# Kernel tuning notes

Hardware: AMD Instinct MI355X
Metric: run time of the kernel (lower is better)

Reference implementation:

```python
import jax, jax.numpy as jnp
import numpy as np

VOCAB, EMBED, HIDDEN, NUM_CLASSES, PAD_IDX = 50257, 128, 128, 4, 0
B, T = 256, 512


def setup_inputs() -> dict:
    key = jax.random.key(0)
    ks = jax.random.split(key, 10)
    x = jax.random.randint(ks[0], (B, T), 0, VOCAB)
    h0 = jnp.zeros((B, HIDDEN), dtype=jnp.float32)
    # embedding: uniform(-0.1, 0.1), pad row zeroed (matches init_weights)
    emb = jax.random.uniform(ks[1], (VOCAB, EMBED), jnp.float32, -0.1, 0.1)
    emb = emb.at[PAD_IDX].set(0.0)
    def xavier(k, shape):
        fan_out, fan_in = shape
        bound = float(np.sqrt(6.0 / (fan_in + fan_out)))
        return jax.random.uniform(k, shape, jnp.float32, -bound, bound)
    W_ih = xavier(ks[2], (HIDDEN, EMBED))      # rnn.weight_ih_l0
    W_hh = xavier(ks[3], (HIDDEN, HIDDEN))     # rnn.weight_hh_l0
    b_ih = jnp.zeros((HIDDEN,), jnp.float32)
    b_hh = jnp.zeros((HIDDEN,), jnp.float32)
    W1 = xavier(ks[4], (2 * HIDDEN, HIDDEN))   # output_layer1
    b1 = jnp.zeros((2 * HIDDEN,), jnp.float32)
    W2 = xavier(ks[5], (NUM_CLASSES, 2 * HIDDEN))  # output_layer2
    b2 = jnp.zeros((NUM_CLASSES,), jnp.float32)
    return {"x": x, "h0": h0, "emb": emb, "W_ih": W_ih, "W_hh": W_hh,
            "b_ih": b_ih, "b_hh": b_hh, "W1": W1, "b1": b1, "W2": W2, "b2": b2}


def reference(x, h0, emb, W_ih, W_hh, b_ih, b_hh, W1, b1, W2, b2):
    # Embedding lookup (dropout layers are identity in eval mode)
    embedded = emb[x]                                    # [B, T, E]
    # Precompute input projection for every step, then scan the recurrence.
    x_proj = jnp.einsum('bte,he->bth', embedded, W_ih) + b_ih + b_hh  # [B, T, H]
    x_proj_t = jnp.swapaxes(x_proj, 0, 1)                # [T, B, H]

    def step(h, xp):
        h_new = jnp.tanh(xp + h @ W_hh.T)                # [B, H]
        return h_new, None

    last_hidden, _ = jax.lax.scan(step, h0, x_proj_t)    # [B, H]
    # MLP head: Linear -> ReLU -> Linear
    hidden_mlp = jax.nn.relu(last_hidden @ W1.T + b1)    # [B, 2H]
    logits = hidden_mlp @ W2.T + b2                      # [B, C]
    return (logits, last_hidden)
```

## Files before the change

kernel.cpp:

```cpp
#include <hip/hip_runtime.h>
#include <hip/hip_bf16.h>
#include <math.h>

#define BB 256
#define TT 512
#define EE 128
#define HH 128
#define NC 4
#define MM (BB * TT)

typedef __bf16 bf16x8 __attribute__((ext_vector_type(8)));
typedef __bf16 bf16x4 __attribute__((ext_vector_type(4)));
typedef float  f32x4  __attribute__((ext_vector_type(4)));
typedef float  f32x2  __attribute__((ext_vector_type(2)));

__device__ __forceinline__ float fast_tanh(float x) {
    float t = __builtin_amdgcn_exp2f(x * 2.885390081777927f);
    return 1.f - 2.f * __builtin_amdgcn_rcpf(1.f + t);
}

template <typename XPT>
__global__ __launch_bounds__(256, 2) void embed_gemm(
    const int* __restrict__ x, const float* __restrict__ emb,
    const float* __restrict__ Wih, const float* __restrict__ bih,
    const float* __restrict__ bhh, XPT* __restrict__ xpout)
{
    const int tid = threadIdx.x;
    const int m0  = blockIdx.x * 128;

    const int LDA = 72;
    __shared__ __bf16 Ah[128 * 72];
    __shared__ __bf16 Al[128 * 72];
    __shared__ __bf16 Wh[128 * 72];
    __shared__ __bf16 Wl[128 * 72];
    __shared__ float  bias_s[128];
    __shared__ int    gix[128];

    if (tid < 128) {
        gix[tid]    = x[m0 + tid];
        bias_s[tid] = bih[tid] + bhh[tid];
    }

    const int lane = tid & 63, wid = tid >> 6;
    const int col  = lane & 15, quad = lane >> 4;

    f32x4 acc[2][8];
#pragma unroll
    for (int mt = 0; mt < 2; ++mt)
#pragma unroll
        for (int nt = 0; nt < 8; ++nt) acc[mt][nt] = f32x4{0.f, 0.f, 0.f, 0.f};

    __syncthreads();

#pragma unroll
    for (int half = 0; half < 2; ++half) {
#pragma unroll
        for (int it = 0; it < 8; ++it) {
            int c   = it * 256 + tid;
            int row = c >> 4;
            int seg = c & 15;

            float4 wv = ((const float4*)Wih)[row * 32 + half * 16 + seg];
            bf16x4 wh, wl;
            wh[0] = (__bf16)wv.x; wl[0] = (__bf16)(wv.x - (float)wh[0]);
            wh[1] = (__bf16)wv.y; wl[1] = (__bf16)(wv.y - (float)wh[1]);
            wh[2] = (__bf16)wv.z; wl[2] = (__bf16)(wv.z - (float)wh[2]);
            wh[3] = (__bf16)wv.w; wl[3] = (__bf16)(wv.w - (float)wh[3]);
            *(bf16x4*)&Wh[row * LDA + seg * 4] = wh;
            *(bf16x4*)&Wl[row * LDA + seg * 4] = wl;

            int gi = gix[row];
            float4 av = ((const float4*)emb)[(size_t)gi * 32 + half * 16 + seg];
            bf16x4 ah, al;
            ah[0] = (__bf16)av.x; al[0] = (__bf16)(av.x - (float)ah[0]);
            ah[1] = (__bf16)av.y; al[1] = (__bf16)(av.y - (float)ah[1]);
            ah[2] = (__bf16)av.z; al[2] = (__bf16)(av.z - (float)ah[2]);
            ah[3] = (__bf16)av.w; al[3] = (__bf16)(av.w - (float)ah[3]);
            *(bf16x4*)&Ah[row * LDA + seg * 4] = ah;
            *(bf16x4*)&Al[row * LDA + seg * 4] = al;
        }
        __syncthreads();

#pragma unroll
        for (int kk = 0; kk < 2; ++kk) {
            bf16x8 afh[2], afl[2];
#pragma unroll
            for (int mt = 0; mt < 2; ++mt) {
                int ro = (wid * 32 + mt * 16 + col) * LDA + kk * 32 + quad * 8;
                afh[mt] = *(const bf16x8*)&Ah[ro];
                afl[mt] = *(const bf16x8*)&Al[ro];
            }
#pragma unroll
            for (int nt = 0; nt < 8; ++nt) {
                int ro = (nt * 16 + col) * LDA + kk * 32 + quad * 8;
                bf16x8 wfh = *(const bf16x8*)&Wh[ro];
                bf16x8 wfl = *(const bf16x8*)&Wl[ro];
#pragma unroll
                for (int mt = 0; mt < 2; ++mt) {
                    acc[mt][nt] = __builtin_amdgcn_mfma_f32_16x16x32_bf16(afh[mt], wfh, acc[mt][nt], 0, 0, 0);
                    acc[mt][nt] = __builtin_amdgcn_mfma_f32_16x16x32_bf16(afl[mt], wfh, acc[mt][nt], 0, 0, 0);
                    acc[mt][nt] = __builtin_amdgcn_mfma_f32_16x16x32_bf16(afh[mt], wfl, acc[mt][nt], 0, 0, 0);
                }
            }
        }
        if (half == 0) __syncthreads();
    }

#pragma unroll
    for (int mt = 0; mt < 2; ++mt) {
#pragma unroll
        for (int nt = 0; nt < 8; ++nt) {
            int m = m0 + wid * 32 + mt * 16 + quad * 4;
            int n = nt * 16 + col;
            float bs = bias_s[n];
#pragma unroll
            for (int r = 0; r < 4; ++r)
                xpout[(size_t)(m + r) * 128 + n] = (XPT)(acc[mt][nt][r] + bs);
        }
    }
}

template <typename XPT>
__global__ __launch_bounds__(256, 1) void rnn_scan(
    const XPT* __restrict__ xp, const float* __restrict__ Whh,
    const float* __restrict__ h0, float* __restrict__ hlast)
{
    const int b    = blockIdx.x;
    const int tid  = threadIdx.x;
    const int q    = tid >> 6;
    const int lane = tid & 63;

    __shared__ float h_s[128];
    __shared__ float part[4 * 128];

    f32x4 wA[8], wB[8];
    {
        const float* r0 = Whh + (size_t)lane * 128 + q * 32;
        const float* r1 = Whh + (size_t)(lane + 64) * 128 + q * 32;
#pragma unroll
        for (int c = 0; c < 8; ++c) {
            wA[c] = *(const f32x4*)(r0 + c * 4);
            wB[c] = *(const f32x4*)(r1 + c * 4);
        }
    }
#pragma unroll
    for (int c = 0; c < 8; ++c)
        asm volatile("" : "+v"(wA[c]), "+v"(wB[c]));

    if (tid < 128) h_s[tid] = h0[b * 128 + tid];

    const XPT* xpb = xp + (size_t)b * (TT * 128);
    float xv[8];
#pragma unroll
    for (int s = 0; s < 8; ++s)
        xv[s] = (tid < 128) ? (float)xpb[s * 128 + tid] : 0.f;
    __syncthreads();

    for (int tw = 0; tw < TT; tw += 8) {
#pragma unroll
        for (int ts = 0; ts < 8; ++ts) {
            const float* hq = &h_s[q * 32];
            f32x4 h4[8];
#pragma unroll
            for (int u = 0; u < 8; ++u) h4[u] = *(const f32x4*)&hq[u * 4];

            f32x4 aA = f32x4{0.f, 0.f, 0.f, 0.f};
            f32x4 aB = f32x4{0.f, 0.f, 0.f, 0.f};
#pragma unroll
            for (int u = 0; u < 8; ++u) {
                aA += wA[u] * h4[u];
                aB += wB[u] * h4[u];
            }
            part[q * 128 + lane]      = (aA[0] + aA[1]) + (aA[2] + aA[3]);
            part[q * 128 + 64 + lane] = (aB[0] + aB[1]) + (aB[2] + aB[3]);
            __syncthreads();
            if (tid < 128) {
                float s = (part[tid] + part[128 + tid])
                        + (part[256 + tid] + part[384 + tid]);
                h_s[tid] = fast_tanh(s + xv[ts]);
                if (tw + 8 < TT)
                    xv[ts] = (float)xpb[(size_t)(tw + 8 + ts) * 128 + tid];
            }
            __syncthreads();
        }
    }
    if (tid < 128) hlast[b * 128 + tid] = h_s[tid];
}

__global__ __launch_bounds__(256, 2) void mlp_head(
    const float* __restrict__ hlast, const float* __restrict__ W1,
    const float* __restrict__ b1, const float* __restrict__ W2,
    const float* __restrict__ b2, float* __restrict__ out)
{
    const int b = blockIdx.x, tid = threadIdx.x;
    __shared__ float h_row[128];
    __shared__ float hid[256];

    if (tid < 128) {
        float hv = hlast[b * 128 + tid];
        h_row[tid] = hv;
        out[1024 + b * 128 + tid] = hv;
    }
    __syncthreads();

    {
        float acc = b1[tid];
        const float4* wrow = (const float4*)(W1 + (size_t)tid * 128);
#pragma unroll
        for (int k4 = 0; k4 < 32; ++k4) {
            float4 wv = wrow[k4];
            acc += wv.x * h_row[k4 * 4 + 0] + wv.y * h_row[k4 * 4 + 1]
                 + wv.z * h_row[k4 * 4 + 2] + wv.w * h_row[k4 * 4 + 3];
        }
        hid[tid] = fmaxf(acc, 0.f);
    }
    __syncthreads();

    const int wv = tid >> 6, lane = tid & 63;
    float s = 0.f;
#pragma unroll
    for (int qq = 0; qq < 4; ++qq)
        s += hid[qq * 64 + lane] * W2[wv * 256 + qq * 64 + lane];
#pragma unroll
    for (int off = 32; off > 0; off >>= 1) s += __shfl_down(s, off);
    if (lane == 0) out[b * 4 + wv] = s + b2[wv];
}

extern "C" void kernel_launch(void* const* d_in, const int* in_sizes, int n_in,
                              void* d_out, int out_size, void* d_ws, size_t ws_size,
                              hipStream_t stream)
{
    const int*   x   = (const int*)d_in[0];
    const float* h0  = (const float*)d_in[1];
    const float* emb = (const float*)d_in[2];
    const float* Wih = (const float*)d_in[3];
    const float* Whh = (const float*)d_in[4];
    const float* bih = (const float*)d_in[5];
    const float* bhh = (const float*)d_in[6];
    const float* W1  = (const float*)d_in[7];
    const float* b1  = (const float*)d_in[8];
    const float* W2  = (const float*)d_in[9];
    const float* b2  = (const float*)d_in[10];
    float* out = (float*)d_out;

    const size_t xp_f32_bytes = (size_t)MM * 128 * sizeof(float);
    const size_t hl_bytes     = (size_t)BB * 128 * sizeof(float);

    if (ws_size >= xp_f32_bytes + hl_bytes) {
        float* xpw = (float*)d_ws;
        float* hl  = (float*)((char*)d_ws + xp_f32_bytes);
        embed_gemm<float><<<MM / 128, 256, 0, stream>>>(x, emb, Wih, bih, bhh, xpw);
        rnn_scan<float><<<BB, 256, 0, stream>>>(xpw, Whh, h0, hl);
        mlp_head<<<BB, 256, 0, stream>>>(hl, W1, b1, W2, b2, out);
    } else {
        __bf16* xpw = (__bf16*)d_ws;
        float*  hl  = (float*)((char*)d_ws + (size_t)MM * 128 * sizeof(__bf16));
        embed_gemm<__bf16><<<MM / 128, 256, 0, stream>>>(x, emb, Wih, bih, bhh, xpw);
        rnn_scan<__bf16><<<BB, 256, 0, stream>>>(xpw, Whh, h0, hl);
        mlp_head<<<BB, 256, 0, stream>>>(hl, W1, b1, W2, b2, out);
    }
}
```

Baseline: 274.3 us.

## Restructure RNN scan reduction with wave shuffles and double-buffered hidden state

Changes the per-step work split so each wave owns 32 output rows, with the two 64-wide K halves held by the two half-waves. The partial dot products are combined with a cross-lane shuffle instead of through a shared-memory partial array. The hidden state is double-buffered, so each timestep needs one block barrier instead of two. The cost is more h reads from LDS per lane per step (64 floats instead of 32), and the xp prefetch is now duplicated across half-waves.

After: 285.3 us. 4.0% more time.

```diff
diff --git a/kernel.cpp b/kernel.cpp
--- a/kernel.cpp
+++ b/kernel.cpp
@@ -127,64 +127,60 @@
 {
     const int b    = blockIdx.x;
     const int tid  = threadIdx.x;
-    const int q    = tid >> 6;
+    const int w    = tid >> 6;
     const int lane = tid & 63;
-
-    __shared__ float h_s[128];
-    __shared__ float part[4 * 128];
-
-    f32x4 wA[8], wB[8];
+    const int o    = lane & 31;
+    const int kh   = lane >> 5;
+
+    __shared__ float h_s[2][128];
+
+    f32x4 wv[16];
     {
-        const float* r0 = Whh + (size_t)lane * 128 + q * 32;
-        const float* r1 = Whh + (size_t)(lane + 64) * 128 + q * 32;
-#pragma unroll
-        for (int c = 0; c < 8; ++c) {
-            wA[c] = *(const f32x4*)(r0 + c * 4);
-            wB[c] = *(const f32x4*)(r1 + c * 4);
-        }
-    }
-#pragma unroll
-    for (int c = 0; c < 8; ++c)
-        asm volatile("" : "+v"(wA[c]), "+v"(wB[c]));
-
-    if (tid < 128) h_s[tid] = h0[b * 128 + tid];
-
-    const XPT* xpb = xp + (size_t)b * (TT * 128);
+        const float* r = Whh + (size_t)(w * 32 + o) * 128 + kh * 64;
+#pragma unroll
+        for (int c = 0; c < 16; ++c) wv[c] = *(const f32x4*)(r + c * 4);
+    }
+#pragma unroll
+    for (int c = 0; c < 16; ++c) asm volatile("" : "+v"(wv[c]));
+
+    if (tid < 128) h_s[0][tid] = h0[b * 128 + tid];
+
+    const XPT* xpb  = xp + (size_t)b * (TT * 128);
+    const int  xoff = w * 32 + o;
     float xv[8];
 #pragma unroll
-    for (int s = 0; s < 8; ++s)
-        xv[s] = (tid < 128) ? (float)xpb[s * 128 + tid] : 0.f;
-    __syncthreads();
-
+    for (int s = 0; s < 8; ++s) xv[s] = (float)xpb[s * 128 + xoff];
+    __syncthreads();
+
+    int cur = 0;
     for (int tw = 0; tw < TT; tw += 8) {
 #pragma unroll
         for (int ts = 0; ts < 8; ++ts) {
-            const float* hq = &h_s[q * 32];
-            f32x4 h4[8];
-#pragma unroll
-            for (int u = 0; u < 8; ++u) h4[u] = *(const f32x4*)&hq[u * 4];
+            const float* hq = &h_s[cur][kh * 64];
+            f32x4 h4[16];
+#pragma unroll
+            for (int u = 0; u < 16; ++u) h4[u] = *(const f32x4*)&hq[u * 4];
 
             f32x4 aA = f32x4{0.f, 0.f, 0.f, 0.f};
             f32x4 aB = f32x4{0.f, 0.f, 0.f, 0.f};
 #pragma unroll
             for (int u = 0; u < 8; ++u) {
-                aA += wA[u] * h4[u];
-                aB += wB[u] * h4[u];
+                aA += wv[u]     * h4[u];
+                aB += wv[u + 8] * h4[u + 8];
             }
-            part[q * 128 + lane]      = (aA[0] + aA[1]) + (aA[2] + aA[3]);
-            part[q * 128 + 64 + lane] = (aB[0] + aB[1]) + (aB[2] + aB[3]);
+            f32x4 at = aA + aB;
+            float p  = (at[0] + at[1]) + (at[2] + at[3]);
+            p += __shfl_xor(p, 32, 64);
+            float hnew = fast_tanh(p + xv[ts]);
+
+            if (lane < 32) h_s[cur ^ 1][w * 32 + o] = hnew;
+            if (tw + 8 < TT)
+                xv[ts] = (float)xpb[(size_t)(tw + 8 + ts) * 128 + xoff];
             __syncthreads();
-            if (tid < 128) {
-                float s = (part[tid] + part[128 + tid])
-                        + (part[256 + tid] + part[384 + tid]);
-                h_s[tid] = fast_tanh(s + xv[ts]);
-                if (tw + 8 < TT)
-                    xv[ts] = (float)xpb[(size_t)(tw + 8 + ts) * 128 + tid];
-            }
-            __syncthreads();
-        }
-    }
-    if (tid < 128) hlast[b * 128 + tid] = h_s[tid];
+            cur ^= 1;
+        }
+    }
+    if (tid < 128) hlast[b * 128 + tid] = h_s[cur][tid];
 }
 
 __global__ __launch_bounds__(256, 2) void mlp_head(
```
